# Optimization experiments

Hardware: AMD Instinct MI355X
Metric: run time of the kernel (lower is better)

Reference implementation:

```python
import jax, jax.numpy as jnp
import numpy as np

NFIELD = 40

def setup_inputs() -> dict:
    key = jax.random.key(0)
    ks = jax.random.split(key, 7)
    B, F, E, A = 1024, NFIELD, 128, 128
    s = 1.0 / np.sqrt(E)
    return {
        "x": jax.random.normal(ks[0], (B, F, E), dtype=jnp.float32),
        "attn_w_w": jax.random.normal(ks[1], (A, E), dtype=jnp.float32) * s,
        "attn_w_b": jax.random.normal(ks[2], (A,), dtype=jnp.float32) * s,
        "attn_h_w": jax.random.normal(ks[3], (1, A), dtype=jnp.float32) * s,
        "attn_h_b": jax.random.normal(ks[4], (1,), dtype=jnp.float32) * s,
        "attn_p_w": jax.random.normal(ks[5], (1, E), dtype=jnp.float32) * s,
        "attn_p_b": jax.random.normal(ks[6], (1,), dtype=jnp.float32) * s,
    }

def reference(x, attn_w_w, attn_w_b, attn_h_w, attn_h_b, attn_p_w, attn_p_b):
    # x: [B, F, E]; pairwise field interactions over upper-triangular (i<j) pairs
    nfield = x.shape[1]
    vi, vj = np.triu_indices(nfield, k=1)  # static index arrays, P = F*(F-1)/2
    hp = x[:, vi, :] * x[:, vj, :]                                   # [B, P, E]
    aw = jax.nn.relu(jnp.einsum('bpe,ae->bpa', hp, attn_w_w) + attn_w_b)  # [B, P, A]
    scores = jnp.einsum('bpa,oa->bpo', aw, attn_h_w) + attn_h_b          # [B, P, 1]
    attn = jax.nn.softmax(scores, axis=1)                                # softmax over pairs
    afm = jnp.sum(attn * hp, axis=1)                                     # [B, E]
    out = jnp.einsum('be,oe->bo', afm, attn_p_w) + attn_p_b              # [B, 1]
    return out.squeeze(1)                                                # [B]
```

## Files before the change

### kernel.cpp

```cpp
#include <hip/hip_runtime.h>
#include <hip/hip_fp16.h>

#define NF 40
#define NE 128
#define NA 128
#define NP 780
#define NPT 784
#define NMT 49
#define XS_LD 132
#define XS16_LD 136
#define G16_LD 72

typedef _Float16 half8 __attribute__((ext_vector_type(8)));
typedef float floatx4 __attribute__((ext_vector_type(4)));

__device__ __forceinline__ float rowsum16(float x) {
    x += __int_as_float(__builtin_amdgcn_update_dpp(0, __float_as_int(x), 0x121, 0xf, 0xf, true));
    x += __int_as_float(__builtin_amdgcn_update_dpp(0, __float_as_int(x), 0x122, 0xf, 0xf, true));
    x += __int_as_float(__builtin_amdgcn_update_dpp(0, __float_as_int(x), 0x124, 0xf, 0xf, true));
    x += __int_as_float(__builtin_amdgcn_update_dpp(0, __float_as_int(x), 0x128, 0xf, 0xf, true));
    return x;
}

__global__ __launch_bounds__(256)
void afm_prep_kernel(const float* __restrict__ wg,
                     unsigned short* __restrict__ wbf,
                     int* __restrict__ ijg)
{
    const int t = blockIdx.x * 256 + threadIdx.x;
    if (t < NA * NE / 4) {
        float4 v = *(const float4*)(wg + t * 4);
        union { _Float16 h[4]; ushort4 u; } c;
        c.h[0] = (_Float16)v.x;
        c.h[1] = (_Float16)v.y;
        c.h[2] = (_Float16)v.z;
        c.h[3] = (_Float16)v.w;
        *(ushort4*)(wbf + t * 4) = c.u;
    }
    if (t < NPT) {
        int v = 0;
        if (t < NP) {
            int i = 0, rem = t;
            while (rem >= (NF - 1 - i)) { rem -= (NF - 1 - i); ++i; }
            v = (i << 8) | (i + 1 + rem);
        }
        ijg[t] = v;
    }
}

__global__ __launch_bounds__(256, 2)
void afm_fused_kernel(const float* __restrict__ xg,
                      const unsigned short* __restrict__ wbf,
                      const int* __restrict__ ijg,
                      const float* __restrict__ wbg,
                      const float* __restrict__ hg,
                      const float* __restrict__ pwg,
                      const float* __restrict__ pbg,
                      float* __restrict__ out)
{
    __shared__ float          xs[NF][XS_LD];
    __shared__ unsigned short xs16[NF][XS16_LD];
    __shared__ int      ij[NPT];
    __shared__ _Float16 G16[48][G16_LD];
    __shared__ float    afm1[NE];
    __shared__ float red_sum[4], red_out[2];

    const int tid  = threadIdx.x;
    const int b    = blockIdx.x;
    const int lane = tid & 63;
    const int wid  = tid >> 6;
    const int col  = lane & 15;
    const int quad = (lane >> 4) & 3;

    for (int t = tid; t < 48 * G16_LD / 2; t += 256)
        ((unsigned*)&G16[0][0])[t] = 0u;

    const float* xb = xg + (size_t)b * (NF * NE);
    for (int t = tid; t < NF * (NE / 4); t += 256) {
        int row = t >> 5, c = (t & 31) * 4;
        float4 v = *(const float4*)(xb + row * NE + c);
        *(float4*)&xs[row][c] = v;
        union { _Float16 h[4]; unsigned long long ull; } cv;
        cv.h[0] = (_Float16)v.x;
        cv.h[1] = (_Float16)v.y;
        cv.h[2] = (_Float16)v.z;
        cv.h[3] = (_Float16)v.w;
        *(unsigned long long*)&xs16[row][c] = cv.ull;
    }
    if (tid < NPT / 4) {
        *(int4*)&ij[tid * 4] = ((const int4*)ijg)[tid];
    }
    float wbr[8], hr[8];
#pragma unroll
    for (int n = 0; n < 8; ++n) {
        wbr[n] = wbg[n * 16 + col];
        hr[n]  = hg[n * 16 + col];
    }
    half8 bfrag[8][4];
#pragma unroll
    for (int n = 0; n < 8; ++n)
#pragma unroll
        for (int k = 0; k < 4; ++k)
            bfrag[n][k] = *(const half8*)(const void*)(wbf + (n * 16 + col) * NE + k * 32 + quad * 8);
    __syncthreads();

    float esum = 0.f;
    for (int mt = wid; mt < NMT; mt += 4) {
        const int p0 = mt * 16;
        const int v  = ij[p0 + col];
        const unsigned short* xi16 = &xs16[(v >> 8) & 255][0];
        const unsigned short* xj16 = &xs16[v & 255][0];

        floatx4 acc[8];
#pragma unroll
        for (int n = 0; n < 8; ++n)
            acc[n] = (floatx4){wbr[n], wbr[n], wbr[n], wbr[n]};

#pragma unroll
        for (int k = 0; k < 4; ++k) {
            const int koff = k * 32 + quad * 8;
            half8 ih = *(const half8*)(const void*)(xi16 + koff);
            half8 jh = *(const half8*)(const void*)(xj16 + koff);
            half8 af = ih * jh;
#pragma unroll
            for (int n = 0; n < 8; ++n)
                acc[n] = __builtin_amdgcn_mfma_f32_16x16x32_f16(af, bfrag[n][k], acc[n], 0, 0, 0);
        }

        float ps[4] = {0.f, 0.f, 0.f, 0.f};
#pragma unroll
        for (int n = 0; n < 8; ++n) {
#pragma unroll
            for (int r = 0; r < 4; ++r)
                ps[r] += fmaxf(acc[n][r], 0.f) * hr[n];
        }
#pragma unroll
        for (int r = 0; r < 4; ++r) ps[r] = rowsum16(ps[r]);

#pragma unroll
        for (int r = 0; r < 4; ++r) {
            const int p = p0 + quad * 4 + r;
            const float e = __expf(ps[r]);
            if (col == 0 && p < NP) {
                const int vv = ij[p];
                const _Float16 eh = (_Float16)e;
                G16[(vv >> 8) & 255][vv & 255] = eh;
                G16[vv & 255][(vv >> 8) & 255] = eh;
                esum += e;
            }
        }
    }
#pragma unroll
    for (int off = 1; off < 64; off <<= 1) esum += __shfl_xor(esum, off);
    if (lane == 0) red_sum[wid] = esum;
    __syncthreads();

    {
        const int n0 = wid * 2;
        float af0 = 0.f, af1 = 0.f;
#pragma unroll
        for (int mt = 0; mt < 3; ++mt) {
            const int arow = mt * 16 + col;
            half8 a1 = *(const half8*)(const void*)&G16[arow][quad * 8];
            half8 a2 = *(const half8*)(const void*)&G16[arow][32 + quad * 8];
#pragma unroll
            for (int nt = 0; nt < 2; ++nt) {
                const int ecol = (n0 + nt) * 16 + col;
                union { half8 h; unsigned short u[8]; } b1, b2;
#pragma unroll
                for (int j = 0; j < 8; ++j)
                    b1.u[j] = xs16[quad * 8 + j][ecol];
#pragma unroll
                for (int j = 0; j < 8; ++j)
                    b2.u[j] = 0;
                if (quad == 0) {
#pragma unroll
                    for (int j = 0; j < 8; ++j)
                        b2.u[j] = xs16[32 + j][ecol];
                }
                floatx4 y = (floatx4){0.f, 0.f, 0.f, 0.f};
                y = __builtin_amdgcn_mfma_f32_16x16x32_f16(a1, b1.h, y, 0, 0, 0);
                y = __builtin_amdgcn_mfma_f32_16x16x32_f16(a2, b2.h, y, 0, 0, 0);
                if (mt * 16 + quad * 4 < NF) {
                    float acc = 0.f;
#pragma unroll
                    for (int r = 0; r < 4; ++r)
                        acc += xs[mt * 16 + quad * 4 + r][ecol] * y[r];
                    if (nt == 0) af0 += acc; else af1 += acc;
                }
            }
        }
        af0 += __shfl_xor(af0, 16);  af0 += __shfl_xor(af0, 32);
        af1 += __shfl_xor(af1, 16);  af1 += __shfl_xor(af1, 32);
        if (lane < 16) {
            afm1[(n0 + 0) * 16 + lane] = af0 * 0.5f;
            afm1[(n0 + 1) * 16 + lane] = af1 * 0.5f;
        }
    }
    __syncthreads();

    float vv = 0.f;
    if (tid < NE) vv = afm1[tid] * pwg[tid];
#pragma unroll
    for (int off = 1; off < 64; off <<= 1) vv += __shfl_xor(vv, off);
    if (lane == 0 && wid < 2) red_out[wid] = vv;
    __syncthreads();
    if (tid == 0) {
        float S   = red_sum[0] + red_sum[1] + red_sum[2] + red_sum[3];
        float tot = red_out[0] + red_out[1];
        out[b] = tot / S + pbg[0];
    }
}

extern "C" void kernel_launch(void* const* d_in, const int* in_sizes, int n_in,
                              void* d_out, int out_size, void* d_ws, size_t ws_size,
                              hipStream_t stream) {
    const float* xg  = (const float*)d_in[0];
    const float* wg  = (const float*)d_in[1];
    const float* wbg = (const float*)d_in[2];
    const float* hg  = (const float*)d_in[3];
    const float* pwg = (const float*)d_in[5];
    const float* pbg = (const float*)d_in[6];
    const int B = in_sizes[0] / (NF * NE);

    unsigned short* wbf = (unsigned short*)d_ws;
    int* ijg = (int*)((char*)d_ws + NA * NE * sizeof(unsigned short));

    afm_prep_kernel<<<16, 256, 0, stream>>>(wg, wbf, ijg);
    afm_fused_kernel<<<B, 256, 0, stream>>>(xg, wbf, ijg, wbg, hg, pwg, pbg, (float*)d_out);
}
```

Before: 119.3 us.

## Fold projection vector into attention GEMM as extra column tile

```diff
diff --git a/kernel.cpp b/kernel.cpp
--- a/kernel.cpp
+++ b/kernel.cpp
@@ -4,12 +4,11 @@
 #define NF 40
 #define NE 128
 #define NA 128
+#define NW 144
 #define NP 780
 #define NPT 784
 #define NMT 49
-#define XS_LD 132
 #define XS16_LD 136
-#define G16_LD 72
 
 typedef _Float16 half8 __attribute__((ext_vector_type(8)));
 typedef float floatx4 __attribute__((ext_vector_type(4)));
@@ -24,18 +23,23 @@
 
 __global__ __launch_bounds__(256)
 void afm_prep_kernel(const float* __restrict__ wg,
+                     const float* __restrict__ pwg,
                      unsigned short* __restrict__ wbf,
                      int* __restrict__ ijg)
 {
     const int t = blockIdx.x * 256 + threadIdx.x;
-    if (t < NA * NE / 4) {
-        float4 v = *(const float4*)(wg + t * 4);
-        union { _Float16 h[4]; ushort4 u; } c;
-        c.h[0] = (_Float16)v.x;
-        c.h[1] = (_Float16)v.y;
-        c.h[2] = (_Float16)v.z;
-        c.h[3] = (_Float16)v.w;
-        *(ushort4*)(wbf + t * 4) = c.u;
+    if (t < NW * NE / 4) {
+        const int row = t >> 5;
+        const int c   = (t & 31) * 4;
+        float4 v = make_float4(0.f, 0.f, 0.f, 0.f);
+        if (row < NA)       v = *(const float4*)(wg + row * NE + c);
+        else if (row == NA) v = *(const float4*)(pwg + c);
+        union { _Float16 h[4]; ushort4 u; } cv;
+        cv.h[0] = (_Float16)v.x;
+        cv.h[1] = (_Float16)v.y;
+        cv.h[2] = (_Float16)v.z;
+        cv.h[3] = (_Float16)v.w;
+        *(ushort4*)(wbf + t * 4) = cv.u;
     }
     if (t < NPT) {
         int v = 0;
@@ -54,16 +58,12 @@
                       const int* __restrict__ ijg,
                       const float* __restrict__ wbg,
                       const float* __restrict__ hg,
-                      const float* __restrict__ pwg,
                       const float* __restrict__ pbg,
                       float* __restrict__ out)
 {
-    __shared__ float          xs[NF][XS_LD];
     __shared__ unsigned short xs16[NF][XS16_LD];
-    __shared__ int      ij[NPT];
-    __shared__ _Float16 G16[48][G16_LD];
-    __shared__ float    afm1[NE];
-    __shared__ float red_sum[4], red_out[2];
+    __shared__ int   ij[NPT];
+    __shared__ float red_n[4], red_d[4];
 
     const int tid  = threadIdx.x;
     const int b    = blockIdx.x;
@@ -72,14 +72,10 @@
     const int col  = lane & 15;
     const int quad = (lane >> 4) & 3;
 
-    for (int t = tid; t < 48 * G16_LD / 2; t += 256)
-        ((unsigned*)&G16[0][0])[t] = 0u;
-
     const float* xb = xg + (size_t)b * (NF * NE);
     for (int t = tid; t < NF * (NE / 4); t += 256) {
         int row = t >> 5, c = (t & 31) * 4;
         float4 v = *(const float4*)(xb + row * NE + c);
-        *(float4*)&xs[row][c] = v;
         union { _Float16 h[4]; unsigned long long ull; } cv;
         cv.h[0] = (_Float16)v.x;
         cv.h[1] = (_Float16)v.y;
@@ -96,25 +92,26 @@
         wbr[n] = wbg[n * 16 + col];
         hr[n]  = hg[n * 16 + col];
     }
-    half8 bfrag[8][4];
+    half8 bfrag[9][4];
 #pragma unroll
-    for (int n = 0; n < 8; ++n)
+    for (int n = 0; n < 9; ++n)
 #pragma unroll
         for (int k = 0; k < 4; ++k)
             bfrag[n][k] = *(const half8*)(const void*)(wbf + (n * 16 + col) * NE + k * 32 + quad * 8);
     __syncthreads();
 
-    float esum = 0.f;
+    float nloc = 0.f, dloc = 0.f;
     for (int mt = wid; mt < NMT; mt += 4) {
         const int p0 = mt * 16;
         const int v  = ij[p0 + col];
         const unsigned short* xi16 = &xs16[(v >> 8) & 255][0];
         const unsigned short* xj16 = &xs16[v & 255][0];
 
-        floatx4 acc[8];
+        floatx4 acc[9];
 #pragma unroll
         for (int n = 0; n < 8; ++n)
             acc[n] = (floatx4){wbr[n], wbr[n], wbr[n], wbr[n]};
+        acc[8] = (floatx4){0.f, 0.f, 0.f, 0.f};
 
 #pragma unroll
         for (int k = 0; k < 4; ++k) {
@@ -123,7 +120,7 @@
             half8 jh = *(const half8*)(const void*)(xj16 + koff);
             half8 af = ih * jh;
 #pragma unroll
-            for (int n = 0; n < 8; ++n)
+            for (int n = 0; n < 9; ++n)
                 acc[n] = __builtin_amdgcn_mfma_f32_16x16x32_f16(af, bfrag[n][k], acc[n], 0, 0, 0);
         }
 
@@ -141,74 +138,24 @@
         for (int r = 0; r < 4; ++r) {
             const int p = p0 + quad * 4 + r;
             const float e = __expf(ps[r]);
-            if (col == 0 && p < NP) {
-                const int vv = ij[p];
-                const _Float16 eh = (_Float16)e;
-                G16[(vv >> 8) & 255][vv & 255] = eh;
-                G16[vv & 255][(vv >> 8) & 255] = eh;
-                esum += e;
+            const bool valid = (col == 0) & (p < NP);
+            if (valid) {
+                nloc += e * acc[8][r];
+                dloc += e;
             }
         }
     }
 #pragma unroll
-    for (int off = 1; off < 64; off <<= 1) esum += __shfl_xor(esum, off);
-    if (lane == 0) red_sum[wid] = esum;
-    __syncthreads();
-
-    {
-        const int n0 = wid * 2;
-        float af0 = 0.f, af1 = 0.f;
-#pragma unroll
-        for (int mt = 0; mt < 3; ++mt) {
-            const int arow = mt * 16 + col;
-            half8 a1 = *(const half8*)(const void*)&G16[arow][quad * 8];
-            half8 a2 = *(const half8*)(const void*)&G16[arow][32 + quad * 8];
-#pragma unroll
-            for (int nt = 0; nt < 2; ++nt) {
-                const int ecol = (n0 + nt) * 16 + col;
-                union { half8 h; unsigned short u[8]; } b1, b2;
-#pragma unroll
-                for (int j = 0; j < 8; ++j)
-                    b1.u[j] = xs16[quad * 8 + j][ecol];
-#pragma unroll
-                for (int j = 0; j < 8; ++j)
-                    b2.u[j] = 0;
-                if (quad == 0) {
-#pragma unroll
-                    for (int j = 0; j < 8; ++j)
-                        b2.u[j] = xs16[32 + j][ecol];
-                }
-                floatx4 y = (floatx4){0.f, 0.f, 0.f, 0.f};
-                y = __builtin_amdgcn_mfma_f32_16x16x32_f16(a1, b1.h, y, 0, 0, 0);
-                y = __builtin_amdgcn_mfma_f32_16x16x32_f16(a2, b2.h, y, 0, 0, 0);
-                if (mt * 16 + quad * 4 < NF) {
-                    float acc = 0.f;
-#pragma unroll
-                    for (int r = 0; r < 4; ++r)
-                        acc += xs[mt * 16 + quad * 4 + r][ecol] * y[r];
-                    if (nt == 0) af0 += acc; else af1 += acc;
-                }
-            }
-        }
-        af0 += __shfl_xor(af0, 16);  af0 += __shfl_xor(af0, 32);
-        af1 += __shfl_xor(af1, 16);  af1 += __shfl_xor(af1, 32);
-        if (lane < 16) {
-            afm1[(n0 + 0) * 16 + lane] = af0 * 0.5f;
-            afm1[(n0 + 1) * 16 + lane] = af1 * 0.5f;
-        }
+    for (int off = 1; off < 64; off <<= 1) {
+        nloc += __shfl_xor(nloc, off);
+        dloc += __shfl_xor(dloc, off);
     }
-    __syncthreads();
-
-    float vv = 0.f;
-    if (tid < NE) vv = afm1[tid] * pwg[tid];
-#pragma unroll
-    for (int off = 1; off < 64; off <<= 1) vv += __shfl_xor(vv, off);
-    if (lane == 0 && wid < 2) red_out[wid] = vv;
+    if (lane == 0) { red_n[wid] = nloc; red_d[wid] = dloc; }
     __syncthreads();
     if (tid == 0) {
-        float S   = red_sum[0] + red_sum[1] + red_sum[2] + red_sum[3];
-        float tot = red_out[0] + red_out[1];
-        out[b] = tot / S + pbg[0];
+        float N = red_n[0] + red_n[1] + red_n[2] + red_n[3];
+        float D = red_d[0] + red_d[1] + red_d[2] + red_d[3];
+        out[b] = N / D + pbg[0];
     }
 }
 
@@ -224,8 +171,8 @@
     const int B = in_sizes[0] / (NF * NE);
 
     unsigned short* wbf = (unsigned short*)d_ws;
-    int* ijg = (int*)((char*)d_ws + NA * NE * sizeof(unsigned short));
+    int* ijg = (int*)((char*)d_ws + NW * NE * sizeof(unsigned short));
 
-    afm_prep_kernel<<<16, 256, 0, stream>>>(wg, wbf, ijg);
-    afm_fused_kernel<<<B, 256, 0, stream>>>(xg, wbf, ijg, wbg, hg, pwg, pbg, (float*)d_out);
+    afm_prep_kernel<<<20, 256, 0, stream>>>(wg, pwg, wbf, ijg);
+    afm_fused_kernel<<<B, 256, 0, stream>>>(xg, wbf, ijg, wbg, hg, pbg, (float*)d_out);
 }
```

Result: faster. 112.3 us (-5.9%).
